# Kernel tuning notes

Measured on AMD Instinct MI355X. Metric: run time of the kernel, lower is better.

Reference implementation:

```python
import jax, jax.numpy as jnp
import numpy as np

KERNEL = 3  # unfold kernel size (stride 1, no padding)

def _unfold(x, k):
    # torch.nn.Unfold(kernel_size=k) equivalent: (B, C, H, W) -> (B, C*k*k, L)
    # channel ordering: index = c*k*k + i*k + j (channel outermost), matching torch.
    B, C, H, W = x.shape
    Ho, Wo = H - k + 1, W - k + 1
    cols = [x[:, :, i:i + Ho, j:j + Wo] for i in range(k) for j in range(k)]  # k*k x (B,C,Ho,Wo)
    u = jnp.stack(cols, axis=2)  # (B, C, k*k, Ho, Wo)
    return u.reshape(B, C * k * k, Ho * Wo)


def setup_inputs() -> dict:
    key = jax.random.key(0)
    k1, k2, k3, k4 = jax.random.split(key, 4)
    B, C, H, W = 512, 3, 64, 64
    M = 512            # num_neurons
    K = C * KERNEL * KERNEL   # input_dim = 27
    L = (H - KERNEL + 1) * (W - KERNEL + 1)  # 3844 patches
    O = 10             # output_dim
    x = jax.random.normal(k1, (B, C, H, W), dtype=jnp.float32)
    G = jax.random.normal(k2, (M, L), dtype=jnp.float32)
    # original inits v,w to zeros; use randn for a non-degenerate reference
    v = jax.random.normal(k3, (M, K, O), dtype=jnp.float32) * 0.02
    w = jax.random.normal(k4, (M, K, O), dtype=jnp.float32) * 0.02
    return {"x": x, "G": G, "v": v, "w": w}


def reference(x, G, v, w):
    # Faithful to:
    #   U = unfold(x)                         (B, K, L)
    #   t = einsum('mn,ikn->imnk', G, U)      (B, M, L, K)  <- never materialized here
    #   out = einsum('ijkl,jlm->im', t, v-w)  (B, O)
    # Reordered as two small contractions (same math, no huge intermediate):
    U = _unfold(x, KERNEL)                    # (B, K, L)
    A = jnp.einsum('bkn,mn->bmk', U, G)       # (B, M, K): contract over patches L
    p_diff = v - w                            # (M, K, O)
    out = jnp.einsum('bmk,mko->bo', A, p_diff)  # (B, O)
    return out
```

## Files before the change

kernel.cpp:

```cpp
#include <hip/hip_runtime.h>
#include <hip/hip_bf16.h>

#define ODIM   10
#define HOg    62
#define LDIM   3844
#define CHW    12288
#define BATCH  512
#define KO     270
#define KOP    272
#define MDIM   512
#define GTN    3904

typedef __attribute__((ext_vector_type(8))) short bfrag;
typedef __attribute__((ext_vector_type(4))) float f32x4;

__global__ __launch_bounds__(256)
void pdt_kernel(const float* __restrict__ v, const float* __restrict__ w,
                __hip_bfloat16* __restrict__ Pdt) {
    int idx = blockIdx.x * 256 + threadIdx.x;
    if (idx >= MDIM * KOP) return;
    int m  = idx / KOP;
    int ko = idx - m * KOP;
    float val = (ko < KO) ? (v[m * KO + ko] - w[m * KO + ko]) : 0.f;
    Pdt[(size_t)ko * MDIM + m] = __float2bfloat16(val);
}

__global__ __launch_bounds__(256)
void gt_kernel(const float* __restrict__ G, __hip_bfloat16* __restrict__ Gt) {
    __shared__ float tile[64][65];
    const int n0 = blockIdx.x * 64;
    const int m0 = blockIdx.y * 64;
    const int tc = threadIdx.x & 63;
    const int tr = threadIdx.x >> 6;

#pragma unroll
    for (int rr = 0; rr < 64; rr += 4) {
        int n = n0 + tc;
        tile[rr + tr][tc] = (n < LDIM) ? G[(size_t)(m0 + rr + tr) * LDIM + n] : 0.f;
    }
    __syncthreads();

    const int nr = threadIdx.x >> 2;
    const int ms = (threadIdx.x & 3) * 16;
    __hip_bfloat16 buf[16];
#pragma unroll
    for (int i = 0; i < 16; ++i)
        buf[i] = __float2bfloat16(tile[ms + i][nr]);
    __hip_bfloat16* dst = Gt + (size_t)(n0 + nr) * MDIM + m0 + ms;
    *reinterpret_cast<uint4*>(dst)     = *reinterpret_cast<uint4*>(&buf[0]);
    *reinterpret_cast<uint4*>(dst + 8) = *reinterpret_cast<uint4*>(&buf[8]);
}

__global__ __launch_bounds__(256)
void tmfma_kernel(const __hip_bfloat16* __restrict__ Pdt,
                  const __hip_bfloat16* __restrict__ Gt,
                  float* __restrict__ T) {
    const int bid   = blockIdx.x;
    const int xcd   = bid & 7;
    const int inner = bid >> 3;
    const int sthi  = inner & 1;
    const int kt    = inner >> 1;
    const int st    = xcd + 8 * sthi;

    const int wv   = threadIdx.x >> 6;
    const int lane = threadIdx.x & 63;
    const int tile = st * 4 + wv;
    if (tile >= 61) return;

    const int n0  = tile * 64;
    const int ko0 = kt * 16;
    const int row = lane & 15;
    const int kg  = lane >> 4;

    const __hip_bfloat16* Ap = Pdt + (size_t)(ko0 + row) * MDIM + kg * 8;
    const __hip_bfloat16* Bp = Gt  + (size_t)(n0 + row) * MDIM + kg * 8;

    f32x4 acc[4];
#pragma unroll
    for (int j = 0; j < 4; ++j) acc[j] = (f32x4){0.f, 0.f, 0.f, 0.f};

#pragma unroll 2
    for (int ks = 0; ks < 16; ++ks) {
        bfrag a = *reinterpret_cast<const bfrag*>(Ap + ks * 32);
#pragma unroll
        for (int j = 0; j < 4; ++j) {
            bfrag b = *reinterpret_cast<const bfrag*>(Bp + (size_t)j * 16 * MDIM + ks * 32);
            acc[j] = __builtin_amdgcn_mfma_f32_16x16x32_bf16(a, b, acc[j], 0, 0, 0);
        }
    }

#pragma unroll
    for (int j = 0; j < 4; ++j) {
        int col = n0 + j * 16 + row;
        if (col < LDIM) {
#pragma unroll
            for (int r = 0; r < 4; ++r) {
                int ro = ko0 + kg * 4 + r;
                if (ro < KO)
                    T[(size_t)ro * LDIM + col] = acc[j][r];
            }
        }
    }
}

__global__ __launch_bounds__(256)
void fold_kernel(const float* __restrict__ T, float* __restrict__ S) {
    int idx = blockIdx.x * 256 + threadIdx.x;
    if (idx >= ODIM * CHW) return;
    int o   = idx / CHW;
    int chw = idx - o * CHW;
    int c = chw >> 12;
    int h = (chw >> 6) & 63;
    int w = chw & 63;

    float s = 0.f;
    for (int i = 0; i < 3; ++i) {
        int pi = h - i;
        if ((unsigned)pi >= HOg) continue;
        for (int j = 0; j < 3; ++j) {
            int pj = w - j;
            if ((unsigned)pj >= HOg) continue;
            int ko = (c * 9 + i * 3 + j) * ODIM + o;
            s += T[(size_t)ko * LDIM + pi * HOg + pj];
        }
    }
    S[idx] = s;
}

__global__ __launch_bounds__(256)
void out_gemm_kernel(const float* __restrict__ X,
                     const float* __restrict__ S,
                     float* __restrict__ out) {
    const int b0  = blockIdx.x * 2;
    const int tid = threadIdx.x;
    const int NV  = CHW / 4;
    const float4* X0 = reinterpret_cast<const float4*>(X) + (size_t)b0 * NV;
    const float4* X1 = X0 + NV;
    const float4* S4 = reinterpret_cast<const float4*>(S);

    float acc0[ODIM], acc1[ODIM];
#pragma unroll
    for (int o = 0; o < ODIM; ++o) { acc0[o] = 0.f; acc1[o] = 0.f; }

    for (int i = tid; i < NV; i += 256) {
        float4 a = X0[i];
        float4 b = X1[i];
#pragma unroll
        for (int o = 0; o < ODIM; ++o) {
            float4 sv = S4[(size_t)o * NV + i];
            acc0[o] += a.x * sv.x + a.y * sv.y + a.z * sv.z + a.w * sv.w;
            acc1[o] += b.x * sv.x + b.y * sv.y + b.z * sv.z + b.w * sv.w;
        }
    }

#pragma unroll
    for (int o = 0; o < ODIM; ++o) {
        float s0 = acc0[o], s1 = acc1[o];
        for (int off = 32; off > 0; off >>= 1) {
            s0 += __shfl_down(s0, off, 64);
            s1 += __shfl_down(s1, off, 64);
        }
        acc0[o] = s0; acc1[o] = s1;
    }

    __shared__ float red[4][2 * ODIM];
    int wave = tid >> 6;
    int lane = tid & 63;
    if (lane == 0) {
#pragma unroll
        for (int o = 0; o < ODIM; ++o) {
            red[wave][o] = acc0[o];
            red[wave][ODIM + o] = acc1[o];
        }
    }
    __syncthreads();
    if (tid < 2 * ODIM) {
        float tsum = red[0][tid] + red[1][tid] + red[2][tid] + red[3][tid];
        int bt = tid / ODIM;
        int o  = tid - bt * ODIM;
        out[(size_t)(b0 + bt) * ODIM + o] = tsum;
    }
}

extern "C" void kernel_launch(void* const* d_in, const int* in_sizes, int n_in,
                              void* d_out, int out_size, void* d_ws, size_t ws_size,
                              hipStream_t stream) {
    const float* x = (const float*)d_in[0];
    const float* G = (const float*)d_in[1];
    const float* v = (const float*)d_in[2];
    const float* w = (const float*)d_in[3];
    float* out = (float*)d_out;

    char* wsb = (char*)d_ws;
    float*          T   = (float*)wsb;
    __hip_bfloat16* Gt  = (__hip_bfloat16*)(wsb + 4151520);
    __hip_bfloat16* Pdt = (__hip_bfloat16*)(wsb + 4151520 + 3997696);
    float*          S   = (float*)(wsb + 4151520 + 3997696 + 278528);

    pdt_kernel<<<(MDIM * KOP + 255) / 256, 256, 0, stream>>>(v, w, Pdt);

    gt_kernel<<<dim3(61, 8), 256, 0, stream>>>(G, Gt);

    tmfma_kernel<<<272, 256, 0, stream>>>(Pdt, Gt, T);

    fold_kernel<<<(ODIM * CHW + 255) / 256, 256, 0, stream>>>(T, S);

    out_gemm_kernel<<<BATCH / 2, 256, 0, stream>>>(x, S, out);
}
```

Measured before the change: 51.95 us.

## Merge prep kernels and fold via atomic scatter from MFMA epilogue

```diff
diff --git a/kernel.cpp b/kernel.cpp
--- a/kernel.cpp
+++ b/kernel.cpp
@@ -9,52 +9,56 @@
 #define KO     270
 #define KOP    272
 #define MDIM   512
-#define GTN    3904
 
 typedef __attribute__((ext_vector_type(8))) short bfrag;
 typedef __attribute__((ext_vector_type(4))) float f32x4;
 
 __global__ __launch_bounds__(256)
-void pdt_kernel(const float* __restrict__ v, const float* __restrict__ w,
-                __hip_bfloat16* __restrict__ Pdt) {
-    int idx = blockIdx.x * 256 + threadIdx.x;
-    if (idx >= MDIM * KOP) return;
-    int m  = idx / KOP;
-    int ko = idx - m * KOP;
-    float val = (ko < KO) ? (v[m * KO + ko] - w[m * KO + ko]) : 0.f;
-    Pdt[(size_t)ko * MDIM + m] = __float2bfloat16(val);
-}
-
-__global__ __launch_bounds__(256)
-void gt_kernel(const float* __restrict__ G, __hip_bfloat16* __restrict__ Gt) {
-    __shared__ float tile[64][65];
-    const int n0 = blockIdx.x * 64;
-    const int m0 = blockIdx.y * 64;
-    const int tc = threadIdx.x & 63;
-    const int tr = threadIdx.x >> 6;
-
-#pragma unroll
-    for (int rr = 0; rr < 64; rr += 4) {
-        int n = n0 + tc;
-        tile[rr + tr][tc] = (n < LDIM) ? G[(size_t)(m0 + rr + tr) * LDIM + n] : 0.f;
-    }
-    __syncthreads();
-
-    const int nr = threadIdx.x >> 2;
-    const int ms = (threadIdx.x & 3) * 16;
-    __hip_bfloat16 buf[16];
-#pragma unroll
-    for (int i = 0; i < 16; ++i)
-        buf[i] = __float2bfloat16(tile[ms + i][nr]);
-    __hip_bfloat16* dst = Gt + (size_t)(n0 + nr) * MDIM + m0 + ms;
-    *reinterpret_cast<uint4*>(dst)     = *reinterpret_cast<uint4*>(&buf[0]);
-    *reinterpret_cast<uint4*>(dst + 8) = *reinterpret_cast<uint4*>(&buf[8]);
+void prep_kernel(const float* __restrict__ G,
+                 const float* __restrict__ v, const float* __restrict__ w,
+                 __hip_bfloat16* __restrict__ Gt,
+                 __hip_bfloat16* __restrict__ Pdt,
+                 float* __restrict__ S) {
+    const int b = blockIdx.x;
+    if (b < 488) {
+        __shared__ float tile[64][65];
+        const int nTile = b % 61;
+        const int mTile = b / 61;
+        const int n0 = nTile * 64;
+        const int m0 = mTile * 64;
+        const int tc = threadIdx.x & 63;
+        const int tr = threadIdx.x >> 6;
+#pragma unroll
+        for (int rr = 0; rr < 64; rr += 4) {
+            int n = n0 + tc;
+            tile[rr + tr][tc] = (n < LDIM) ? G[(size_t)(m0 + rr + tr) * LDIM + n] : 0.f;
+        }
+        __syncthreads();
+        const int nr = threadIdx.x >> 2;
+        const int ms = (threadIdx.x & 3) * 16;
+        __hip_bfloat16 buf[16];
+#pragma unroll
+        for (int i = 0; i < 16; ++i)
+            buf[i] = __float2bfloat16(tile[ms + i][nr]);
+        __hip_bfloat16* dst = Gt + (size_t)(n0 + nr) * MDIM + m0 + ms;
+        *reinterpret_cast<uint4*>(dst)     = *reinterpret_cast<uint4*>(&buf[0]);
+        *reinterpret_cast<uint4*>(dst + 8) = *reinterpret_cast<uint4*>(&buf[8]);
+    } else if (b < 1032) {
+        int idx = (b - 488) * 256 + threadIdx.x;
+        int m  = idx / KOP;
+        int ko = idx - m * KOP;
+        float val = (ko < KO) ? (v[m * KO + ko] - w[m * KO + ko]) : 0.f;
+        Pdt[(size_t)ko * MDIM + m] = __float2bfloat16(val);
+    } else {
+        int idx = (b - 1032) * 256 + threadIdx.x;
+        S[idx] = 0.f;
+    }
 }
 
 __global__ __launch_bounds__(256)
 void tmfma_kernel(const __hip_bfloat16* __restrict__ Pdt,
                   const __hip_bfloat16* __restrict__ Gt,
-                  float* __restrict__ T) {
+                  float* __restrict__ S) {
     const int bid   = blockIdx.x;
     const int xcd   = bid & 7;
     const int inner = bid >> 3;
@@ -75,56 +79,53 @@
     const __hip_bfloat16* Ap = Pdt + (size_t)(ko0 + row) * MDIM + kg * 8;
     const __hip_bfloat16* Bp = Gt  + (size_t)(n0 + row) * MDIM + kg * 8;
 
+    bfrag a[16];
+#pragma unroll
+    for (int ks = 0; ks < 16; ++ks)
+        a[ks] = *reinterpret_cast<const bfrag*>(Ap + ks * 32);
+
     f32x4 acc[4];
 #pragma unroll
     for (int j = 0; j < 4; ++j) acc[j] = (f32x4){0.f, 0.f, 0.f, 0.f};
 
-#pragma unroll 2
+#pragma unroll 4
     for (int ks = 0; ks < 16; ++ks) {
-        bfrag a = *reinterpret_cast<const bfrag*>(Ap + ks * 32);
 #pragma unroll
         for (int j = 0; j < 4; ++j) {
-            bfrag b = *reinterpret_cast<const bfrag*>(Bp + (size_t)j * 16 * MDIM + ks * 32);
-            acc[j] = __builtin_amdgcn_mfma_f32_16x16x32_bf16(a, b, acc[j], 0, 0, 0);
-        }
-    }
-
+            bfrag bfr = *reinterpret_cast<const bfrag*>(Bp + (size_t)j * 16 * MDIM + ks * 32);
+            acc[j] = __builtin_amdgcn_mfma_f32_16x16x32_bf16(a[ks], bfr, acc[j], 0, 0, 0);
+        }
+    }
+
+    int sbase[4];
+    bool kval[4];
+#pragma unroll
+    for (int r = 0; r < 4; ++r) {
+        int ko = ko0 + kg * 4 + r;
+        kval[r] = (ko < KO);
+        int kc  = kval[r] ? ko : 0;
+        int o   = kc % ODIM;
+        int rem = kc / ODIM;
+        int c   = rem / 9;
+        int ij  = rem - c * 9;
+        int i   = ij / 3;
+        int jk  = ij - i * 3;
+        sbase[r] = o * CHW + c * 4096 + i * 64 + jk;
+    }
 #pragma unroll
     for (int j = 0; j < 4; ++j) {
         int col = n0 + j * 16 + row;
         if (col < LDIM) {
+            int pi  = col / HOg;
+            int pj  = col - pi * HOg;
+            int off = pi * 64 + pj;
 #pragma unroll
             for (int r = 0; r < 4; ++r) {
-                int ro = ko0 + kg * 4 + r;
-                if (ro < KO)
-                    T[(size_t)ro * LDIM + col] = acc[j][r];
+                if (kval[r])
+                    atomicAdd(&S[sbase[r] + off], acc[j][r]);
             }
         }
     }
-}
-
-__global__ __launch_bounds__(256)
-void fold_kernel(const float* __restrict__ T, float* __restrict__ S) {
-    int idx = blockIdx.x * 256 + threadIdx.x;
-    if (idx >= ODIM * CHW) return;
-    int o   = idx / CHW;
-    int chw = idx - o * CHW;
-    int c = chw >> 12;
-    int h = (chw >> 6) & 63;
-    int w = chw & 63;
-
-    float s = 0.f;
-    for (int i = 0; i < 3; ++i) {
-        int pi = h - i;
-        if ((unsigned)pi >= HOg) continue;
-        for (int j = 0; j < 3; ++j) {
-            int pj = w - j;
-            if ((unsigned)pj >= HOg) continue;
-            int ko = (c * 9 + i * 3 + j) * ODIM + o;
-            s += T[(size_t)ko * LDIM + pi * HOg + pj];
-        }
-    }
-    S[idx] = s;
 }
 
 __global__ __launch_bounds__(256)
@@ -192,18 +193,13 @@
     float* out = (float*)d_out;
 
     char* wsb = (char*)d_ws;
-    float*          T   = (float*)wsb;
-    __hip_bfloat16* Gt  = (__hip_bfloat16*)(wsb + 4151520);
-    __hip_bfloat16* Pdt = (__hip_bfloat16*)(wsb + 4151520 + 3997696);
-    float*          S   = (float*)(wsb + 4151520 + 3997696 + 278528);
-
-    pdt_kernel<<<(MDIM * KOP + 255) / 256, 256, 0, stream>>>(v, w, Pdt);
-
-    gt_kernel<<<dim3(61, 8), 256, 0, stream>>>(G, Gt);
-
-    tmfma_kernel<<<272, 256, 0, stream>>>(Pdt, Gt, T);
-
-    fold_kernel<<<(ODIM * CHW + 255) / 256, 256, 0, stream>>>(T, S);
+    float*          S   = (float*)wsb;
+    __hip_bfloat16* Gt  = (__hip_bfloat16*)(wsb + 491520);
+    __hip_bfloat16* Pdt = (__hip_bfloat16*)(wsb + 491520 + 3997696);
+
+    prep_kernel<<<1512, 256, 0, stream>>>(G, v, w, Gt, Pdt, S);
+
+    tmfma_kernel<<<272, 256, 0, stream>>>(Pdt, Gt, S);
 
     out_gemm_kernel<<<BATCH / 2, 256, 0, stream>>>(x, S, out);
 }
```

Result: no change. 51.44 us (-1.0%).
